# Kernel tuning notes

Measured on AMD Instinct MI355X. Metric: run time of the kernel, lower is better.

## Reference

```python
import jax, jax.numpy as jnp
import numpy as np

N_NODES = 50000
N_EDGES = 800000
LN_EPS = 1e-5


def _segment_softmax_aggr(msg, t, dst, n):
    # SoftmaxAggregation(learn=True): alpha = softmax(msg * t) per dest segment, out = sum(alpha * msg)
    logits = msg * t  # [E, C]
    m = jax.ops.segment_max(logits, dst, num_segments=n)
    m = jnp.where(jnp.isfinite(m), m, 0.0)  # empty segments -> 0 to keep exp finite
    e = jnp.exp(logits - m[dst])
    denom = jax.ops.segment_sum(e, dst, num_segments=n)
    alpha = e / jnp.maximum(denom[dst], 1e-16)
    return jax.ops.segment_sum(alpha * msg, dst, num_segments=n)


def _sage_conv(x, src, dst, wp, bp, t, wl, bl, wr):
    # project=True: messages come from relu(lin(x)); root term uses ORIGINAL x
    xp = jax.nn.relu(x @ wp + bp)
    msg = xp[src]                                   # [E, C] gather
    aggr = _segment_softmax_aggr(msg, t, dst, x.shape[0])
    out = aggr @ wl + bl + x @ wr
    # normalize=True: L2 normalize rows (eps as in F.normalize)
    nrm = jnp.maximum(jnp.linalg.norm(out, axis=-1, keepdims=True), 1e-12)
    return out / nrm


def _mem_pool(x, k, w_conv, wl, bl):
    # PyG MemPooling, tau=1: Student-t kernel 1/(1+d^2)
    H, K, F = k.shape
    kk = k.reshape(H * K, F)
    d2 = (jnp.sum(kk * kk, -1)[:, None] + jnp.sum(x * x, -1)[None, :]
          - 2.0 * kk @ x.T)                          # [H*K, N]
    d2 = jnp.maximum(d2, 0.0)
    dist = 1.0 / (1.0 + d2)
    dist = dist.reshape(H, K, -1).transpose(0, 2, 1)  # [H, N, K]
    S = dist / jnp.sum(dist, -1, keepdims=True)       # per-head normalize over clusters
    S = jnp.einsum('h,hnk->nk', w_conv, S)            # 1x1 conv mixing heads (no bias)
    S = jax.nn.softmax(S, axis=-1)                    # [N, K]
    xp = S.T @ x                                      # [K, F]
    return xp @ wl + bl                               # [K, out]


def setup_inputs() -> dict:
    key = jax.random.key(0)
    ks = jax.random.split(key, 20)
    rn = lambda i, shp, s: jax.random.normal(ks[i], shp, dtype=jnp.float32) * s
    inp = {
        'x': rn(0, (N_NODES, 64), 1.0),
        'edge_index': jax.random.randint(ks[1], (2, N_EDGES), 0, N_NODES, dtype=jnp.int32),
        'w_proj1': rn(2, (64, 64), 0.1), 'b_proj1': rn(3, (64,), 0.05),
        't1': jnp.ones((64,), jnp.float32),
        'w_l1': rn(4, (64, 256), 0.1), 'b_l1': rn(5, (256,), 0.05),
        'w_r1': rn(6, (64, 256), 0.1),
        'w_proj2': rn(7, (256, 256), 0.05), 'b_proj2': rn(8, (256,), 0.05),
        't2': jnp.ones((256,), jnp.float32),
        'w_l2': rn(9, (256, 128), 0.05), 'b_l2': rn(10, (128,), 0.05),
        'w_r2': rn(11, (256, 128), 0.05),
        'k_mem': rn(12, (4, 4, 128), 1.0),
        'w_conv': rn(13, (4,), 0.5),
        'w_memlin': rn(14, (128, 128), 0.08), 'b_memlin': rn(15, (128,), 0.05),
        'w_fx': rn(16, (128, 64), 0.08), 'b_fx': rn(17, (64,), 0.05),
        'gamma': jnp.ones((64,), jnp.float32),
        'beta': jnp.zeros((64,), jnp.float32),
    }
    return inp


def reference(x, edge_index, w_proj1, b_proj1, t1, w_l1, b_l1, w_r1,
              w_proj2, b_proj2, t2, w_l2, b_l2, w_r2,
              k_mem, w_conv, w_memlin, b_memlin, w_fx, b_fx, gamma, beta):
    src, dst = edge_index[0], edge_index[1]
    h = _sage_conv(x, src, dst, w_proj1, b_proj1, t1, w_l1, b_l1, w_r1)
    h = jax.nn.relu(h)                              # dropout = identity (eval)
    h = _sage_conv(h, src, dst, w_proj2, b_proj2, t2, w_l2, b_l2, w_r2)
    h = jax.nn.relu(h)
    pooled = _mem_pool(h, k_mem, w_conv, w_memlin, b_memlin)  # [4, 128]
    g = jnp.mean(pooled, axis=0, keepdims=True)     # global_mean_pool -> [1, 128]
    y = g @ w_fx + b_fx                             # [1, 64]
    mu = jnp.mean(y, -1, keepdims=True)
    var = jnp.var(y, -1, keepdims=True)
    y = (y - mu) / jnp.sqrt(var + LN_EPS) * gamma + beta
    return jax.nn.relu(y)
```

## Files before the change

kernel.cpp:

```cpp
#include <hip/hip_runtime.h>
#include <hip/hip_bf16.h>

#define N_NODES 50000
#define N_EDGES 800000
#define NB 196
#define NBK 512
#define EPB 1563
#define PC_SLICES 2048
#define NWAVES 8192

typedef __attribute__((ext_vector_type(8))) short short8;
typedef __attribute__((ext_vector_type(4))) float f32x4;
typedef __attribute__((ext_vector_type(2))) float f32x2;

#define QSCALE2 (2.f / 255.f)
#define QINV2   127.5f
#define QSCALE1 (12.75f / 255.f)
#define QINV1   20.f

__device__ __forceinline__ float us2f(unsigned short u) {
    return __uint_as_float(((unsigned int)u) << 16);
}
__device__ __forceinline__ unsigned short f2bu(float f) {
    unsigned int u = __float_as_uint(f);
    unsigned int r = (u + 0x7fffu + ((u >> 16) & 1u)) >> 16;
    return (unsigned short)r;
}
__device__ __forceinline__ float exp2_hw(float x) {
    float r;
    __asm__("v_exp_f32 %0, %1" : "=v"(r) : "v"(x));
    return r;
}
__device__ __forceinline__ void async16(const void* g, void* l) {
    __builtin_amdgcn_global_load_lds(
        (const __attribute__((address_space(1))) unsigned int*)g,
        (__attribute__((address_space(3))) unsigned int*)l, 16, 0, 0);
}
#define LOG2E 1.44269504088896f

__global__ __launch_bounds__(256) void k_bhist(const int* __restrict__ dst,
                                               int* __restrict__ counts,
                                               int* __restrict__ bcnt) {
    __shared__ int h[196];
    int t = threadIdx.x, b = blockIdx.x;
    if (t < 196) h[t] = 0;
    __syncthreads();
    int e0 = b * EPB, e1 = e0 + EPB < N_EDGES ? e0 + EPB : N_EDGES;
    for (int e = e0 + t; e < e1; e += 256) {
        int d = dst[e];
        atomicAdd(&h[d >> 8], 1);
        atomicAdd(&counts[d], 1);
    }
    __syncthreads();
    if (t < 196) bcnt[b * 196 + t] = h[t];
}

__global__ __launch_bounds__(256) void k_scan1(const int* __restrict__ counts,
                                               int* __restrict__ row_ptr,
                                               int* __restrict__ partial) {
    __shared__ int sd[256];
    int t = threadIdx.x, i = blockIdx.x * 256 + t;
    int v = (i < N_NODES) ? counts[i] : 0;
    sd[t] = v;
    __syncthreads();
    for (int off = 1; off < 256; off <<= 1) {
        int o = (t >= off) ? sd[t - off] : 0;
        __syncthreads();
        sd[t] += o;
        __syncthreads();
    }
    if (i < N_NODES) row_ptr[i] = sd[t] - v;
    if (t == 255) partial[blockIdx.x] = sd[255];
}

__global__ __launch_bounds__(256) void k_scan3b(int* __restrict__ row_ptr,
                                                const int* __restrict__ partial) {
    __shared__ int sd[256];
    int t = threadIdx.x;
    sd[t] = (t < blockIdx.x) ? partial[t] : 0;
    __syncthreads();
    for (int off = 128; off > 0; off >>= 1) {
        if (t < off) sd[t] += sd[t + off];
        __syncthreads();
    }
    int base = sd[0];
    int i = blockIdx.x * 256 + t;
    if (i < N_NODES) row_ptr[i] += base;
    if (blockIdx.x == 0 && t == 0) row_ptr[N_NODES] = N_EDGES;
}

__global__ __launch_bounds__(512) void k_bscan(const int* __restrict__ bcnt,
                                               const int* __restrict__ row_ptr,
                                               int* __restrict__ boff) {
    __shared__ int sd[512];
    int q = blockIdx.x, t = threadIdx.x;
    int v = bcnt[t * 196 + q];
    sd[t] = v;
    __syncthreads();
    for (int off = 1; off < 512; off <<= 1) {
        int o = (t >= off) ? sd[t - off] : 0;
        __syncthreads();
        sd[t] += o;
        __syncthreads();
    }
    boff[t * 196 + q] = row_ptr[q * 256] + sd[t] - v;
}

__global__ __launch_bounds__(256) void k_bucket2(const int* __restrict__ src,
                                                 const int* __restrict__ dst,
                                                 const int* __restrict__ boff,
                                                 int* __restrict__ tmp) {
    __shared__ int lcur[196];
    int t = threadIdx.x, b = blockIdx.x;
    if (t < 196) lcur[t] = boff[b * 196 + t];
    __syncthreads();
    int e0 = b * EPB, e1 = e0 + EPB < N_EDGES ? e0 + EPB : N_EDGES;
    for (int e = e0 + t; e < e1; e += 256) {
        int d = dst[e];
        int pos = atomicAdd(&lcur[d >> 8], 1);
        tmp[pos] = src[e] | ((d & 255) << 16);
    }
}

__global__ __launch_bounds__(256) void k_scatter2(const int* __restrict__ row_ptr,
                                                  const int* __restrict__ tmp,
                                                  int* __restrict__ src_sorted) {
    __shared__ int lcur[256];
    int b = blockIdx.x, t = threadIdx.x;
    int n0 = b * 256;
    int nhi = n0 + 256 < N_NODES ? n0 + 256 : N_NODES;
    if (n0 + t < nhi) lcur[t] = row_ptr[n0 + t];
    __syncthreads();
    int ebeg = row_ptr[n0], eend = row_ptr[nhi];
    for (int i = ebeg + t; i < eend; i += 256) {
        int w = tmp[i];
        int pos = atomicAdd(&lcur[(w >> 16) & 255], 1);
        src_sorted[pos] = w & 0xFFFF;
    }
}

__global__ __launch_bounds__(256) void k_split(const int* __restrict__ row_ptr,
                                               int* __restrict__ split) {
    int w = blockIdx.x * 256 + threadIdx.x;
    if (w > NWAVES) return;
    if (w == NWAVES) { split[w] = N_NODES; return; }
    int target = (int)((long long)w * N_EDGES / NWAVES);
    int lo = 0, hi = N_NODES;
    while (lo < hi) {
        int mid = (lo + hi) >> 1;
        if (row_ptr[mid] < target) lo = mid + 1; else hi = mid;
    }
    split[w] = lo;
}

#define XCAST_N (N_NODES * 64)
#define PREP_TOT (XCAST_N + 167936)
__global__ __launch_bounds__(256) void k_prep(const float* __restrict__ x,
                                              const float* __restrict__ wp1,
                                              const float* __restrict__ wl1,
                                              const float* __restrict__ wr1,
                                              const float* __restrict__ wp2,
                                              const float* __restrict__ wl2,
                                              const float* __restrict__ wr2,
                                              unsigned short* __restrict__ cat1,
                                              unsigned short* __restrict__ B0T,
                                              unsigned short* __restrict__ B1T,
                                              unsigned short* __restrict__ BP2T,
                                              unsigned short* __restrict__ B2T) {
    int idx = (blockIdx.x * 256 + threadIdx.x) * 4;
    if (idx < XCAST_N) {
        int i = idx >> 6, j = idx & 63;
        float4 v = *(const float4*)&x[idx];
        ushort4 o = { f2bu(v.x), f2bu(v.y), f2bu(v.z), f2bu(v.w) };
        *(ushort4*)&cat1[i * 128 + 64 + j] = o;
        return;
    }
    int w = idx - XCAST_N;
    if (w < 4096)  { float4 v = *(const float4*)&wp1[w]; int k = w >> 6, n = w & 63;
                     B0T[n*64+k]=f2bu(v.x); B0T[(n+1)*64+k]=f2bu(v.y);
                     B0T[(n+2)*64+k]=f2bu(v.z); B0T[(n+3)*64+k]=f2bu(v.w); return; }
    w -= 4096;
    if (w < 16384) { float4 v = *(const float4*)&wl1[w]; int k = w >> 8, n = w & 255;
                     B1T[n*128+k]=f2bu(v.x); B1T[(n+1)*128+k]=f2bu(v.y);
                     B1T[(n+2)*128+k]=f2bu(v.z); B1T[(n+3)*128+k]=f2bu(v.w); return; }
    w -= 16384;
    if (w < 16384) { float4 v = *(const float4*)&wr1[w]; int k = w >> 8, n = w & 255;
                     B1T[n*128+64+k]=f2bu(v.x); B1T[(n+1)*128+64+k]=f2bu(v.y);
                     B1T[(n+2)*128+64+k]=f2bu(v.z); B1T[(n+3)*128+64+k]=f2bu(v.w); return; }
    w -= 16384;
    if (w < 65536) { float4 v = *(const float4*)&wp2[w]; int k = w >> 8, n = w & 255;
                     BP2T[n*256+k]=f2bu(v.x); BP2T[(n+1)*256+k]=f2bu(v.y);
                     BP2T[(n+2)*256+k]=f2bu(v.z); BP2T[(n+3)*256+k]=f2bu(v.w); return; }
    w -= 65536;
    if (w < 32768) { float4 v = *(const float4*)&wl2[w]; int k = w >> 7, n = w & 127;
                     B2T[n*512+k]=f2bu(v.x); B2T[(n+1)*512+k]=f2bu(v.y);
                     B2T[(n+2)*512+k]=f2bu(v.z); B2T[(n+3)*512+k]=f2bu(v.w); return; }
    w -= 32768;
    if (w < 32768) { float4 v = *(const float4*)&wr2[w]; int k = w >> 7, n = w & 127;
                     B2T[n*512+256+k]=f2bu(v.x); B2T[(n+1)*512+256+k]=f2bu(v.y);
                     B2T[(n+2)*512+256+k]=f2bu(v.z); B2T[(n+3)*512+256+k]=f2bu(v.w); return; }
}

template<int K, int C, int LDA, int LDOUT, int OUT_OFF, int EP, int WPB, int MH, int PIPE>
__global__ __launch_bounds__(256, WPB) void k_gemm(const unsigned short* __restrict__ A,
                                                   const unsigned short* __restrict__ BT,
                                                   const float* __restrict__ bias,
                                                   void* __restrict__ outv,
                                                   const float* __restrict__ kmem,
                                                   const float* __restrict__ wconv,
                                                   float* __restrict__ Sm,
                                                   float qinv) {
    constexpr int NT = C / 16;
    constexpr int SAE = 64 * MH * 64;
    constexpr int SBE = C * 64;
    constexpr int BUFE = SAE + SBE;
    constexpr int STAGE_B = BUFE * 2 * (PIPE ? 2 : 1);
    constexpr int RPLD = (EP == 2) ? (C + 4) : ((EP == 3) ? (C + 16) : (C + 8));
    constexpr int RP_B = 64 * RPLD * (EP == 2 ? 4 : (EP == 3 ? 1 : 2));
    constexpr int SMEM_B = STAGE_B > RP_B ? STAGE_B : RP_B;
    constexpr int POOL_B = (EP == 2) ? (2048 * 4 + 64 + 16) : 16;
    __shared__ __align__(16) char smem[SMEM_B + POOL_B];
    unsigned short* sA = (unsigned short*)smem;
    float* kls  = (float*)(smem + SMEM_B);
    float* kk2s = kls + 2048;
    float* wcs  = kk2s + 16;

    int t = threadIdx.x;
    int wid = t >> 6, lane = t & 63;
    int lrow = lane & 15, quad = lane >> 4;
    int m0 = blockIdx.x * (64 * MH);

    if (EP == 2) {
        for (int i = t; i < 2048; i += 256) kls[i] = kmem[i];
        if (t < 4) wcs[t] = wconv[t];
        __syncthreads();
        if (t < 16) {
            float s = 0.f;
            for (int f = 0; f < 128; ++f) { float v = kls[t * 128 + f]; s += v * v; }
            kk2s[t] = s;
        }
    }

    f32x4 acc[MH][NT];
#pragma unroll
    for (int h = 0; h < MH; ++h)
#pragma unroll
        for (int nt = 0; nt < NT; ++nt)
#pragma unroll
            for (int r = 0; r < 4; ++r) acc[h][nt][r] = 0.f;

    auto stage = [&](int step, int buf) {
        unsigned short* sAb = sA + buf * BUFE;
        unsigned short* sBb = sAb + SAE;
        int k0 = step * 64;
        for (int i = t; i < 64 * MH * 8; i += 256) {
            int r = i >> 3, seg = i & 7;
            size_t m = (size_t)(m0 + r);
            async16(&A[m * LDA + k0 + ((seg ^ (r & 7)) << 3)],
                    (char*)sAb + (size_t)(i - lane) * 16);
        }
        for (int i = t; i < C * 8; i += 256) {
            int n = i >> 3, seg = i & 7;
            async16(&BT[(size_t)n * K + k0 + ((seg ^ (n & 7)) << 3)],
                    (char*)sBb + (size_t)(i - lane) * 16);
        }
    };
    auto compute = [&](int buf) {
        unsigned short* sAb = sA + buf * BUFE;
        unsigned short* sBb = sAb + SAE;
#pragma unroll
        for (int kk = 0; kk < 2; ++kk) {
            int sw = lrow & 7;
            short8 av[MH];
#pragma unroll
            for (int h = 0; h < MH; ++h)
                av[h] = *(const short8*)&sAb[(h * 64 + wid * 16 + lrow) * 64 +
                                             (((kk * 4 + quad) ^ sw) << 3)];
#pragma unroll
            for (int nt = 0; nt < NT; ++nt) {
                short8 bfg = *(const short8*)&sBb[(nt * 16 + lrow) * 64 +
                                                  (((kk * 4 + quad) ^ sw) << 3)];
#pragma unroll
                for (int h = 0; h < MH; ++h)
                    acc[h][nt] = __builtin_amdgcn_mfma_f32_16x16x32_bf16(av[h], bfg, acc[h][nt], 0, 0, 0);
            }
        }
    };

    constexpr int NSTEP = K / 64;
    if (PIPE) {
        stage(0, 0);
        __syncthreads();
        for (int step = 0; step < NSTEP; ++step) {
            int cur = step & 1;
            if (step + 1 < NSTEP) stage(step + 1, cur ^ 1);
            compute(cur);
            __syncthreads();
        }
    } else {
        for (int step = 0; step < NSTEP; ++step) {
            __syncthreads();
            stage(step, 0);
            __syncthreads();
            compute(0);
        }
    }

#pragma unroll
    for (int h = 0; h < MH; ++h) {
#pragma unroll
        for (int nt = 0; nt < NT; ++nt) {
            float bv = bias[nt * 16 + lrow];
#pragma unroll
            for (int r = 0; r < 4; ++r) acc[h][nt][r] += bv;
        }
        if (EP == 1 || EP == 2) {
#pragma unroll
            for (int r = 0; r < 4; ++r) {
                float ss = 0.f;
#pragma unroll
                for (int nt = 0; nt < NT; ++nt) ss += acc[h][nt][r] * acc[h][nt][r];
                ss += __shfl_xor(ss, 1);
                ss += __shfl_xor(ss, 2);
                ss += __shfl_xor(ss, 4);
                ss += __shfl_xor(ss, 8);
                float rinv = 1.f / fmaxf(sqrtf(ss), 1e-12f);
#pragma unroll
                for (int nt = 0; nt < NT; ++nt)
                    acc[h][nt][r] = fmaxf(acc[h][nt][r] * rinv, 0.f);
            }
        } else {
#pragma unroll
            for (int nt = 0; nt < NT; ++nt)
#pragma unroll
                for (int r = 0; r < 4; ++r) acc[h][nt][r] = fmaxf(acc[h][nt][r], 0.f);
        }
    }

    __syncthreads();
#pragma unroll
    for (int h = 0; h < MH; ++h) {
        if (EP == 2) {
            float* rp = (float*)smem;
#pragma unroll
            for (int nt = 0; nt < NT; ++nt)
#pragma unroll
                for (int r = 0; r < 4; ++r)
                    rp[(wid * 16 + quad * 4 + r) * RPLD + nt * 16 + lrow] = acc[h][nt][r];
            __syncthreads();
            float* outp = (float*)outv;
            for (int i = t; i < 64 * C / 4; i += 256) {
                int f = i * 4, r = f / C, c = f % C;
                int m = m0 + h * 64 + r;
                if (m < N_NODES)
                    *(float4*)&outp[(size_t)m * LDOUT + OUT_OFF + c] = *(const float4*)&rp[r * RPLD + c];
            }
            {
                int row = t >> 2, p = t & 3;
                int cbase = p * 32;
                float dots[16];
#pragma unroll
                for (int k = 0; k < 16; ++k) dots[k] = 0.f;
                float x2 = 0.f;
#pragma unroll
                for (int j = 0; j < 8; ++j) {
                    int c4 = (j + p * 2) & 7;
                    float4 xv = *(const float4*)&rp[row * RPLD + cbase + c4 * 4];
                    x2 += xv.x * xv.x + xv.y * xv.y + xv.z * xv.z + xv.w * xv.w;
#pragma unroll
                    for (int k = 0; k < 16; ++k) {
                        float4 kv = *(const float4*)&kls[k * 128 + cbase + c4 * 4];
                        dots[k] += xv.x * kv.x + xv.y * kv.y + xv.z * kv.z + xv.w * kv.w;
                    }
                }
#pragma unroll
                for (int k = 0; k < 16; ++k) {
                    dots[k] += __shfl_xor(dots[k], 1);
                    dots[k] += __shfl_xor(dots[k], 2);
                }
                x2 += __shfl_xor(x2, 1);
                x2 += __shfl_xor(x2, 2);
                if (p == 0) {
                    int m = m0 + h * 64 + row;
                    if (m < N_NODES) {
                        float dist[16];
#pragma unroll
                        for (int k = 0; k < 16; ++k) {
                            float d2 = fmaxf(kk2s[k] + x2 - 2.f * dots[k], 0.f);
                            dist[k] = 1.f / (1.f + d2);
                        }
                        float s0 = 0.f, s1 = 0.f, s2 = 0.f, s3 = 0.f;
#pragma unroll
                        for (int hh = 0; hh < 4; ++hh) {
                            float den = dist[hh * 4] + dist[hh * 4 + 1] +
                                        dist[hh * 4 + 2] + dist[hh * 4 + 3];
                            float inv = wcs[hh] / den;
                            s0 += dist[hh * 4 + 0] * inv;
                            s1 += dist[hh * 4 + 1] * inv;
                            s2 += dist[hh * 4 + 2] * inv;
                            s3 += dist[hh * 4 + 3] * inv;
                        }
                        float mx = fmaxf(fmaxf(s0, s1), fmaxf(s2, s3));
                        float e0 = __expf(s0 - mx), e1 = __expf(s1 - mx);
                        float e2 = __expf(s2 - mx), e3 = __expf(s3 - mx);
                        float inv = 1.f / (e0 + e1 + e2 + e3);
                        *(float4*)&Sm[(size_t)m * 4] =
                            make_float4(e0 * inv, e1 * inv, e2 * inv, e3 * inv);
                    }
                }
            }
            __syncthreads();
        } else if (EP == 3) {
            unsigned char* rp = (unsigned char*)smem;
#pragma unroll
            for (int nt = 0; nt < NT; ++nt)
#pragma unroll
                for (int r = 0; r < 4; ++r) {
                    float q = fminf(__builtin_rintf(acc[h][nt][r] * qinv), 255.f);
                    rp[(wid * 16 + quad * 4 + r) * RPLD + nt * 16 + lrow] = (unsigned char)(int)q;
                }
            __syncthreads();
            unsigned char* outp = (unsigned char*)outv;
            for (int i = t; i < 64 * C / 16; i += 256) {
                int f = i * 16, r = f / C, c = f % C;
                int m = m0 + h * 64 + r;
                if (m < N_NODES)
                    *(uint4*)&outp[(size_t)m * LDOUT + OUT_OFF + c] = *(const uint4*)&rp[r * RPLD + c];
            }
            __syncthreads();
        } else {
            unsigned short* rp = (unsigned short*)smem;
#pragma unroll
            for (int nt = 0; nt < NT; ++nt)
#pragma unroll
                for (int r = 0; r < 4; ++r)
                    rp[(wid * 16 + quad * 4 + r) * RPLD + nt * 16 + lrow] = f2bu(acc[h][nt][r]);
            __syncthreads();
            unsigned short* outp = (unsigned short*)outv;
            for (int i = t; i < 64 * C / 8; i += 256) {
                int f = i * 8, r = f / C, c = f % C;
                int m = m0 + h * 64 + r;
                if (m < N_NODES)
                    *(uint4*)&outp[(size_t)m * LDOUT + OUT_OFF + c] = *(const uint4*)&rp[r * RPLD + c];
            }
            __syncthreads();
        }
    }
}

__global__ __launch_bounds__(256, 4) void k_aggr256(const unsigned char* __restrict__ xp,
                                                    const float* __restrict__ tvec,
                                                    const int* __restrict__ row_ptr,
                                                    const int* __restrict__ srcs,
                                                    const int* __restrict__ split,
                                                    unsigned short* __restrict__ outp) {
    int t = threadIdx.x & 63;
    int w = blockIdx.x * 4 + (threadIdx.x >> 6);
    float4 tv4 = *(const float4*)&tvec[t * 4];
    f32x2 tv01 = {tv4.x * (LOG2E * QSCALE2), tv4.y * (LOG2E * QSCALE2)};
    f32x2 tv23 = {tv4.z * (LOG2E * QSCALE2), tv4.w * (LOG2E * QSCALE2)};
    int n    = __builtin_amdgcn_readfirstlane(split[w]);
    int nend = __builtin_amdgcn_readfirstlane(split[w + 1]);
    if (n >= nend) return;
    int e    = __builtin_amdgcn_readfirstlane(row_ptr[n]);
    int eend = __builtin_amdgcn_readfirstlane(row_ptr[nend]);
    int rp_next = __builtin_amdgcn_readfirstlane(row_ptr[n + 1]);
    f32x2 se01 = {0.f, 0.f}, se23 = {0.f, 0.f};
    f32x2 sem01 = {0.f, 0.f}, sem23 = {0.f, 0.f};

#define FINALIZE()                                                             \
    {                                                                          \
        ushort4 o;                                                             \
        o.x = f2bu(QSCALE2 * sem01.x / fmaxf(se01.x, 1e-16f));                 \
        o.y = f2bu(QSCALE2 * sem01.y / fmaxf(se01.y, 1e-16f));                 \
        o.z = f2bu(QSCALE2 * sem23.x / fmaxf(se23.x, 1e-16f));                 \
        o.w = f2bu(QSCALE2 * sem23.y / fmaxf(se23.y, 1e-16f));                 \
        *(ushort4*)&outp[(size_t)n * 512 + t * 4] = o;                         \
        se01 = (f32x2){0.f, 0.f}; se23 = (f32x2){0.f, 0.f};                    \
        sem01 = (f32x2){0.f, 0.f}; sem23 = (f32x2){0.f, 0.f};                  \
        ++n;                                                                   \
        rp_next = (n < nend) ? __builtin_amdgcn_readfirstlane(row_ptr[n + 1])  \
                             : 0x7FFFFFFF;                                     \
    }
#define EDGE_BODY(VV)                                                          \
    {                                                                          \
        f32x2 m01 = {(float)((VV) & 0xFFu), (float)(((VV) >> 8) & 0xFFu)};     \
        f32x2 m23 = {(float)(((VV) >> 16) & 0xFFu), (float)((VV) >> 24)};      \
        f32x2 l01 = m01 * tv01, l23 = m23 * tv23;                              \
        f32x2 w01, w23;                                                        \
        w01.x = exp2_hw(l01.x); w01.y = exp2_hw(l01.y);                        \
        w23.x = exp2_hw(l23.x); w23.y = exp2_hw(l23.y);                        \
        se01 += w01; se23 += w23;                                              \
        sem01 = __builtin_elementwise_fma(w01, m01, sem01);                    \
        sem23 = __builtin_elementwise_fma(w23, m23, sem23);                    \
    }

    while (rp_next <= e) FINALIZE();

    while (e < eend) {
        unsigned int v[16];
        int rem = eend - e;
        int cnt = rem > 16 ? 16 : rem;
        if (cnt == 16) {
#pragma unroll
            for (int j = 0; j < 16; ++j) {
                const unsigned char* p = xp + (size_t)srcs[e + j] * 256;
                v[j] = *(const unsigned int*)&p[t * 4];
            }
        } else {
#pragma unroll
            for (int j = 0; j < 16; ++j) {
                int ee = e + j;
                ee = ee < eend ? ee : eend - 1;
                const unsigned char* p = xp + (size_t)srcs[ee] * 256;
                v[j] = *(const unsigned int*)&p[t * 4];
            }
        }
#pragma unroll
        for (int j = 0; j < 16; ++j) {
            if (j < cnt) {
                EDGE_BODY(v[j])
                while (e + j + 1 == rp_next) FINALIZE();
            }
        }
        e += cnt;
    }
#undef EDGE_BODY
#undef FINALIZE
}

__global__ __launch_bounds__(256, 4) void k_aggr64(const unsigned char* __restrict__ xp,
                                                   const float* __restrict__ tvec,
                                                   const int* __restrict__ row_ptr,
                                                   const int* __restrict__ srcs,
                                                   const int* __restrict__ split,
                                                   unsigned short* __restrict__ outp) {
    int c = threadIdx.x & 63;
    int w = blockIdx.x * 4 + (threadIdx.x >> 6);
    float tv = tvec[c] * (LOG2E * QSCALE1);
    int n    = __builtin_amdgcn_readfirstlane(split[w]);
    int nend = __builtin_amdgcn_readfirstlane(split[w + 1]);
    if (n >= nend) return;
    int e    = __builtin_amdgcn_readfirstlane(row_ptr[n]);
    int eend = __builtin_amdgcn_readfirstlane(row_ptr[nend]);
    int rp_next = __builtin_amdgcn_readfirstlane(row_ptr[n + 1]);
    float se = 0.f, sem = 0.f;

#define FIN1()                                                                 \
    {                                                                          \
        outp[(size_t)n * 128 + c] = f2bu(QSCALE1 * sem / fmaxf(se, 1e-16f));   \
        se = 0.f; sem = 0.f;                                                   \
        ++n;                                                                   \
        rp_next = (n < nend) ? __builtin_amdgcn_readfirstlane(row_ptr[n + 1])  \
                             : 0x7FFFFFFF;                                     \
    }

    while (rp_next <= e) FIN1();

    while (e < eend) {
        unsigned char v[16];
        int rem = eend - e;
        int cnt = rem > 16 ? 16 : rem;
        if (cnt == 16) {
#pragma unroll
            for (int j = 0; j < 16; ++j)
                v[j] = xp[(size_t)srcs[e + j] * 64 + c];
        } else {
#pragma unroll
            for (int j = 0; j < 16; ++j) {
                int ee = e + j;
                ee = ee < eend ? ee : eend - 1;
                v[j] = xp[(size_t)srcs[ee] * 64 + c];
            }
        }
#pragma unroll
        for (int j = 0; j < 16; ++j) {
            if (j < cnt) {
                float msg = (float)v[j];
                float wv = exp2_hw(msg * tv);
                se += wv;
                sem = fmaf(wv, msg, sem);
                while (e + j + 1 == rp_next) FIN1();
            }
        }
        e += cnt;
    }
#undef FIN1
}

__global__ __launch_bounds__(256) void k_pool_c(const float* __restrict__ h2,
                                                const float* __restrict__ Sm,
                                                float* __restrict__ part) {
    int t = threadIdx.x;
    int c = t & 127, sub = t >> 7;
    int slice = blockIdx.x * 2 + sub;
    float a0 = 0.f, a1 = 0.f, a2 = 0.f, a3 = 0.f;
    for (int n = slice; n < N_NODES; n += PC_SLICES) {
        float xv = h2[(size_t)n * 128 + c];
        float4 sv = *(const float4*)&Sm[(size_t)n * 4];
        a0 = fmaf(sv.x, xv, a0);
        a1 = fmaf(sv.y, xv, a1);
        a2 = fmaf(sv.z, xv, a2);
        a3 = fmaf(sv.w, xv, a3);
    }
    float* p = &part[(size_t)slice * 512];
    p[0 * 128 + c] = a0;
    p[1 * 128 + c] = a1;
    p[2 * 128 + c] = a2;
    p[3 * 128 + c] = a3;
}

__global__ __launch_bounds__(256) void k_pool_b(const float* __restrict__ part,
                                                float* __restrict__ pooled) {
    int j = blockIdx.x;
    float s = 0.f;
    for (int b = threadIdx.x; b < PC_SLICES; b += 256) s += part[(size_t)b * 512 + j];
#pragma unroll
    for (int off = 32; off > 0; off >>= 1) s += __shfl_xor(s, off);
    __shared__ float red[4];
    int lane = threadIdx.x & 63, wid = threadIdx.x >> 6;
    if (lane == 0) red[wid] = s;
    __syncthreads();
    if (threadIdx.x == 0) pooled[j] = red[0] + red[1] + red[2] + red[3];
}

__global__ __launch_bounds__(128) void k_final(const float* __restrict__ pooled,
                                               const float* __restrict__ wmem,
                                               const float* __restrict__ bmem,
                                               const float* __restrict__ wfx,
                                               const float* __restrict__ bfx,
                                               const float* __restrict__ gamma,
                                               const float* __restrict__ beta,
                                               float* __restrict__ out) {
    __shared__ float gx[128], g[128];
    int t = threadIdx.x;
    gx[t] = 0.25f * (pooled[t] + pooled[128 + t] + pooled[256 + t] + pooled[384 + t]);
    __syncthreads();
    float acc = bmem[t];
    for (int f = 0; f < 128; ++f) acc = fmaf(gx[f], wmem[f * 128 + t], acc);
    g[t] = acc;
    __syncthreads();
    if (t < 64) {
        float y = bfx[t];
        for (int f = 0; f < 128; ++f) y = fmaf(g[f], wfx[f * 64 + t], y);
        float s = y, s2 = y * y;
#pragma unroll
        for (int off = 32; off > 0; off >>= 1) {
            s += __shfl_xor(s, off);
            s2 += __shfl_xor(s2, off);
        }
        float mu = s * (1.f / 64.f);
        float var = s2 * (1.f / 64.f) - mu * mu;
        float v = (y - mu) / sqrtf(var + 1e-5f) * gamma[t] + beta[t];
        out[t] = fmaxf(v, 0.f);
    }
}

extern "C" void kernel_launch(void* const* d_in, const int* in_sizes, int n_in,
                              void* d_out, int out_size, void* d_ws, size_t ws_size,
                              hipStream_t stream) {
    const float* x        = (const float*)d_in[0];
    const int*   ei       = (const int*)  d_in[1];
    const float* w_proj1  = (const float*)d_in[2];
    const float* b_proj1  = (const float*)d_in[3];
    const float* t1       = (const float*)d_in[4];
    const float* w_l1     = (const float*)d_in[5];
    const float* b_l1     = (const float*)d_in[6];
    const float* w_r1     = (const float*)d_in[7];
    const float* w_proj2  = (const float*)d_in[8];
    const float* b_proj2  = (const float*)d_in[9];
    const float* t2       = (const float*)d_in[10];
    const float* w_l2     = (const float*)d_in[11];
    const float* b_l2     = (const float*)d_in[12];
    const float* w_r2     = (const float*)d_in[13];
    const float* k_mem    = (const float*)d_in[14];
    const float* w_conv   = (const float*)d_in[15];
    const float* w_memlin = (const float*)d_in[16];
    const float* b_memlin = (const float*)d_in[17];
    const float* w_fx     = (const float*)d_in[18];
    const float* b_fx     = (const float*)d_in[19];
    const float* gamma    = (const float*)d_in[20];
    const float* beta     = (const float*)d_in[21];
    const int* src = ei;
    const int* dst = ei + N_EDGES;
    (void)in_sizes; (void)n_in; (void)out_size; (void)ws_size;

    char* W = (char*)d_ws;
    const size_t MB = 1024 * 1024;
    int*   row_ptr    = (int*)(W + 0);
    int*   counts     = (int*)(W + 256 * 1024);
    int*   partial    = (int*)(W + 512 * 1024);
    int*   split      = (int*)(W + 520 * 1024);
    int*   src_sorted = (int*)(W + 768 * 1024);
    unsigned short* cat1 = (unsigned short*)(W + 4 * MB);
    unsigned char*  xp1  = (unsigned char*)(W + 17 * MB);
    unsigned short* cat2 = (unsigned short*)(W + 24 * MB);
    unsigned char*  xp2  = (unsigned char*)(W + 76 * MB);
    float* h2     = (float*)(W + 102 * MB);
    float* Sm     = (float*)(W + 128 * MB);
    float* pooled = (float*)(W + 131 * MB);
    unsigned short* B0T  = (unsigned short*)(W + 133 * MB);
    unsigned short* B1T  = (unsigned short*)(W + 134 * MB);
    unsigned short* BP2T = (unsigned short*)(W + 135 * MB);
    unsigned short* B2T  = (unsigned short*)(W + 136 * MB);
    int*   boff   = (int*)(W + 137 * MB);
    int*   bcnt   = (int*)(W + 138 * MB);
    float* part   = (float*)(W + 140 * MB);
    int*   tmp_e  = (int*)(W + 144 * MB);

    hipMemsetAsync(counts, 0, N_NODES * sizeof(int), stream);
    k_bhist<<<NBK, 256, 0, stream>>>(dst, counts, bcnt);
    k_scan1<<<NB, 256, 0, stream>>>(counts, row_ptr, partial);
    k_scan3b<<<NB, 256, 0, stream>>>(row_ptr, partial);
    k_bscan<<<NB, 512, 0, stream>>>(bcnt, row_ptr, boff);
    k_split<<<(NWAVES + 1 + 255) / 256, 256, 0, stream>>>(row_ptr, split);
    k_bucket2<<<NBK, 256, 0, stream>>>(src, dst, boff, tmp_e);
    k_scatter2<<<NB, 256, 0, stream>>>(row_ptr, tmp_e, src_sorted);

    k_prep<<<(PREP_TOT / 4 + 255) / 256, 256, 0, stream>>>(
        x, w_proj1, w_l1, w_r1, w_proj2, w_l2, w_r2, cat1, B0T, B1T, BP2T, B2T);

    const int GB = (N_NODES + 127) / 128;
    const int AGB = NWAVES / 4;

    k_gemm<64, 64, 128, 64, 0, 3, 4, 2, 0><<<GB, 256, 0, stream>>>(
        cat1 + 64, B0T, b_proj1, xp1, nullptr, nullptr, nullptr, QINV1);
    k_aggr64<<<AGB, 256, 0, stream>>>(xp1, t1, row_ptr, src_sorted, split, cat1);
    k_gemm<128, 256, 128, 512, 256, 1, 3, 2, 0><<<GB, 256, 0, stream>>>(
        cat1, B1T, b_l1, cat2, nullptr, nullptr, nullptr, 0.f);

    k_gemm<256, 256, 512, 256, 0, 3, 3, 2, 0><<<GB, 256, 0, stream>>>(
        cat2 + 256, BP2T, b_proj2, xp2, nullptr, nullptr, nullptr, QINV2);
    k_aggr256<<<AGB, 256, 0, stream>>>(xp2, t2, row_ptr, src_sorted, split, cat2);
    k_gemm<512, 128, 512, 128, 0, 2, 3, 2, 1><<<GB, 256, 0, stream>>>(
        cat2, B2T, b_l2, h2, k_mem, w_conv, Sm, 0.f);

    k_pool_c<<<PC_SLICES / 2, 256, 0, stream>>>(h2, Sm, part);
    k_pool_b<<<512, 256, 0, stream>>>(part, pooled);
    k_final<<<1, 128, 0, stream>>>(pooled, w_memlin, b_memlin, w_fx, b_fx, gamma, beta,
                                   (float*)d_out);
}
```

Baseline: 343.7 us.

## Fuse memory-pool S^T·x reduction into final GEMM epilogue, drop h2/Sm round trip

The last GEMM epilogue now accumulates per-block partial sums of S^T·h directly from shared memory instead of writing h2 (50000x128 floats) and Sm to global memory. The separate k_pool_c kernel is removed, and k_pool_b reduces over 391 block partials instead of 2048 slices. This removes a large global write and re-read plus one kernel launch. In exchange the GEMM epilogue gets an extra 64-row serial loop and another barrier per half-tile.

After: 349.4 us. About the same (+1.7%).

```diff
diff --git a/kernel.cpp b/kernel.cpp
--- a/kernel.cpp
+++ b/kernel.cpp
@@ -6,7 +6,7 @@
 #define NB 196
 #define NBK 512
 #define EPB 1563
-#define PC_SLICES 2048
+#define GBLK 391
 #define NWAVES 8192
 
 typedef __attribute__((ext_vector_type(8))) short short8;
@@ -218,12 +218,13 @@
     constexpr int RPLD = (EP == 2) ? (C + 4) : ((EP == 3) ? (C + 16) : (C + 8));
     constexpr int RP_B = 64 * RPLD * (EP == 2 ? 4 : (EP == 3 ? 1 : 2));
     constexpr int SMEM_B = STAGE_B > RP_B ? STAGE_B : RP_B;
-    constexpr int POOL_B = (EP == 2) ? (2048 * 4 + 64 + 16) : 16;
+    constexpr int POOL_B = (EP == 2) ? (2048 * 4 + 64 + 16 + 1024) : 16;
     __shared__ __align__(16) char smem[SMEM_B + POOL_B];
     unsigned short* sA = (unsigned short*)smem;
     float* kls  = (float*)(smem + SMEM_B);
     float* kk2s = kls + 2048;
     float* wcs  = kk2s + 16;
+    float* sS   = wcs + 4;
 
     int t = threadIdx.x;
     int wid = t >> 6, lane = t & 63;
@@ -337,6 +338,8 @@
         }
     }
 
+    float pacc0 = 0.f, pacc1 = 0.f;
+
     __syncthreads();
 #pragma unroll
     for (int h = 0; h < MH; ++h) {
@@ -348,13 +351,6 @@
                 for (int r = 0; r < 4; ++r)
                     rp[(wid * 16 + quad * 4 + r) * RPLD + nt * 16 + lrow] = acc[h][nt][r];
             __syncthreads();
-            float* outp = (float*)outv;
-            for (int i = t; i < 64 * C / 4; i += 256) {
-                int f = i * 4, r = f / C, c = f % C;
-                int m = m0 + h * 64 + r;
-                if (m < N_NODES)
-                    *(float4*)&outp[(size_t)m * LDOUT + OUT_OFF + c] = *(const float4*)&rp[r * RPLD + c];
-            }
             {
                 int row = t >> 2, p = t & 3;
                 int cbase = p * 32;
@@ -382,6 +378,7 @@
                 x2 += __shfl_xor(x2, 2);
                 if (p == 0) {
                     int m = m0 + h * 64 + row;
+                    float4 sv = make_float4(0.f, 0.f, 0.f, 0.f);
                     if (m < N_NODES) {
                         float dist[16];
 #pragma unroll
@@ -404,9 +401,18 @@
                         float e0 = __expf(s0 - mx), e1 = __expf(s1 - mx);
                         float e2 = __expf(s2 - mx), e3 = __expf(s3 - mx);
                         float inv = 1.f / (e0 + e1 + e2 + e3);
-                        *(float4*)&Sm[(size_t)m * 4] =
-                            make_float4(e0 * inv, e1 * inv, e2 * inv, e3 * inv);
+                        sv = make_float4(e0 * inv, e1 * inv, e2 * inv, e3 * inv);
                     }
+                    *(float4*)&sS[row * 4] = sv;
+                }
+            }
+            __syncthreads();
+            {
+                int c = t & 127, kq = t >> 7;
+                for (int r = 0; r < 64; ++r) {
+                    float xv = rp[r * RPLD + c];
+                    pacc0 = fmaf(sS[r * 4 + kq], xv, pacc0);
+                    pacc1 = fmaf(sS[r * 4 + 2 + kq], xv, pacc1);
                 }
             }
             __syncthreads();
@@ -446,6 +452,12 @@
             __syncthreads();
         }
     }
+    if (EP == 2) {
+        float* partp = (float*)outv;
+        partp[(size_t)blockIdx.x * 512 + t] = pacc0;
+        partp[(size_t)blockIdx.x * 512 + 256 + t] = pacc1;
+    }
+    (void)Sm;
 }
 
 __global__ __launch_bounds__(256, 4) void k_aggr256(const unsigned char* __restrict__ xp,
@@ -588,33 +600,11 @@
 #undef FIN1
 }
 
-__global__ __launch_bounds__(256) void k_pool_c(const float* __restrict__ h2,
-                                                const float* __restrict__ Sm,
-                                                float* __restrict__ part) {
-    int t = threadIdx.x;
-    int c = t & 127, sub = t >> 7;
-    int slice = blockIdx.x * 2 + sub;
-    float a0 = 0.f, a1 = 0.f, a2 = 0.f, a3 = 0.f;
-    for (int n = slice; n < N_NODES; n += PC_SLICES) {
-        float xv = h2[(size_t)n * 128 + c];
-        float4 sv = *(const float4*)&Sm[(size_t)n * 4];
-        a0 = fmaf(sv.x, xv, a0);
-        a1 = fmaf(sv.y, xv, a1);
-        a2 = fmaf(sv.z, xv, a2);
-        a3 = fmaf(sv.w, xv, a3);
-    }
-    float* p = &part[(size_t)slice * 512];
-    p[0 * 128 + c] = a0;
-    p[1 * 128 + c] = a1;
-    p[2 * 128 + c] = a2;
-    p[3 * 128 + c] = a3;
-}
-
 __global__ __launch_bounds__(256) void k_pool_b(const float* __restrict__ part,
                                                 float* __restrict__ pooled) {
     int j = blockIdx.x;
     float s = 0.f;
-    for (int b = threadIdx.x; b < PC_SLICES; b += 256) s += part[(size_t)b * 512 + j];
+    for (int b = threadIdx.x; b < GBLK; b += 256) s += part[(size_t)b * 512 + j];
 #pragma unroll
     for (int off = 32; off > 0; off >>= 1) s += __shfl_xor(s, off);
     __shared__ float red[4];
@@ -696,8 +686,6 @@
     unsigned char*  xp1  = (unsigned char*)(W + 17 * MB);
     unsigned short* cat2 = (unsigned short*)(W + 24 * MB);
     unsigned char*  xp2  = (unsigned char*)(W + 76 * MB);
-    float* h2     = (float*)(W + 102 * MB);
-    float* Sm     = (float*)(W + 128 * MB);
     float* pooled = (float*)(W + 131 * MB);
     unsigned short* B0T  = (unsigned short*)(W + 133 * MB);
     unsigned short* B1T  = (unsigned short*)(W + 134 * MB);
@@ -720,7 +708,7 @@
     k_prep<<<(PREP_TOT / 4 + 255) / 256, 256, 0, stream>>>(
         x, w_proj1, w_l1, w_r1, w_proj2, w_l2, w_r2, cat1, B0T, B1T, BP2T, B2T);
 
-    const int GB = (N_NODES + 127) / 128;
+    const int GB = GBLK;
     const int AGB = NWAVES / 4;
 
     k_gemm<64, 64, 128, 64, 0, 3, 4, 2, 0><<<GB, 256, 0, stream>>>(
@@ -733,9 +721,8 @@
         cat2 + 256, BP2T, b_proj2, xp2, nullptr, nullptr, nullptr, QINV2);
     k_aggr256<<<AGB, 256, 0, stream>>>(xp2, t2, row_ptr, src_sorted, split, cat2);
     k_gemm<512, 128, 512, 128, 0, 2, 3, 2, 1><<<GB, 256, 0, stream>>>(
-        cat2, B2T, b_l2, h2, k_mem, w_conv, Sm, 0.f);
-
-    k_pool_c<<<PC_SLICES / 2, 256, 0, stream>>>(h2, Sm, part);
+        cat2, B2T, b_l2, part, k_mem, w_conv, nullptr, 0.f);
+
     k_pool_b<<<512, 256, 0, stream>>>(part, pooled);
     k_final<<<1, 128, 0, stream>>>(pooled, w_memlin, b_memlin, w_fx, b_fx, gamma, beta,
                                    (float*)d_out);
```
